# Kernel optimization log

Hardware: AMD Instinct MI355X
Metric: run time of the kernel (lower is better)

The kernel has to match this reference:

```python
import jax, jax.numpy as jnp
import numpy as np

B, T, D = 2, 2048, 2048
H = 8
KEY_DIM, VAL_DIM = 1024, 2048   # expand_k=0.5, expand_v=1.0
HK, HV = KEY_DIM // H, VAL_DIM // H
LOW_RANK = 16
GATE_NORM = 16.0
CHUNK = 64
HIDDEN = (D * 4 * 2 // 3 + 63) // 64 * 64  # 5504, exactly as GLUFFN.__init__
EPS = 1e-6


def rmsnorm(x, w):
    return x * jax.lax.rsqrt(jnp.mean(x * x, axis=-1, keepdims=True) + EPS) * w


def setup_inputs() -> dict:
    key = jax.random.key(0)
    ks = jax.random.split(key, 12)
    w = lambda k, s: jax.random.normal(k, s, jnp.float32) * 0.02
    return {
        "x": jax.random.normal(ks[0], (B, T, D), jnp.float32),
        "norm1_w": jnp.ones((D,), jnp.float32),
        "wq": w(ks[1], (D, KEY_DIM)),
        "wk": w(ks[2], (D, KEY_DIM)),
        "wv": w(ks[3], (D, VAL_DIM)),
        "gk_w1": w(ks[4], (D, LOW_RANK)),
        "gk_w2": w(ks[5], (LOW_RANK, KEY_DIM)),
        "gk_b": jnp.zeros((KEY_DIM,), jnp.float32),
        "wg": w(ks[6], (D, VAL_DIM)),
        "gnorm_w": jnp.ones((HV,), jnp.float32),
        "wo": w(ks[7], (VAL_DIM, D)),
        "ffn_norm_w": jnp.ones((D,), jnp.float32),
        "w_gate": w(ks[8], (D, HIDDEN)),
        "w_up": w(ks[9], (D, HIDDEN)),
        "w_down": w(ks[10], (HIDDEN, D)),
    }


def _gla(h, wq, wk, wv, gk_w1, gk_w2, gk_b, wg, gnorm_w, wo):
    # Gated linear attention, chunk-parallel form (fla-style):
    #   S_t = diag(exp(g_t)) S_{t-1} + k_t^T v_t ;  o_t = q_t S_t
    Bb, Tt, _ = h.shape
    nc = Tt // CHUNK

    def split(t, hd):  # [B,T,H*hd] -> [nc,B,H,CHUNK,hd]
        t = t.reshape(Bb, nc, CHUNK, H, hd)
        return jnp.transpose(t, (1, 0, 3, 2, 4))

    q = split(h @ wq, HK) * (HK ** -0.5)
    k = split(h @ wk, HK)
    v = split(h @ wv, HV)
    # low-rank forget gate, log-sigmoid scaled by gate_logit_normalizer=16
    g = split(jax.nn.log_sigmoid(h @ gk_w1 @ gk_w2 + gk_b) / GATE_NORM, HK)

    mask = jnp.tril(jnp.ones((CHUNK, CHUNK), jnp.float32))

    def step(S, inp):
        qc, kc, vc, gc = inp                       # [B,H,C,*]
        b = jnp.cumsum(gc, axis=-2)                # cumulative log-decay within chunk
        qe = qc * jnp.exp(b)
        A = jnp.einsum('bhik,bhjk->bhij', qe, kc * jnp.exp(-b)) * mask
        o = jnp.einsum('bhck,bhkv->bhcv', qe, S) + jnp.einsum('bhij,bhjv->bhiv', A, vc)
        bl = b[:, :, -1:, :]                       # decay to end of chunk
        S = jnp.exp(bl[:, :, 0, :])[..., None] * S + \
            jnp.einsum('bhck,bhcv->bhkv', kc * jnp.exp(bl - b), vc)
        return S, o

    S0 = jnp.zeros((Bb, H, HK, HV), h.dtype)
    _, o = jax.lax.scan(step, S0, (q, k, v, g))    # o: [nc,B,H,C,HV]
    o = jnp.transpose(o, (1, 0, 3, 2, 4)).reshape(Bb, Tt, H, HV)

    gate = (h @ wg).reshape(Bb, Tt, H, HV)
    # per-head RMSNorm + swish output gate (FusedRMSNormSwishGate)
    o = rmsnorm(o, gnorm_w) * gate * jax.nn.sigmoid(gate)
    return o.reshape(Bb, Tt, VAL_DIM) @ wo


def reference(x, norm1_w, wq, wk, wv, gk_w1, gk_w2, gk_b, wg, gnorm_w, wo,
              ffn_norm_w, w_gate, w_up, w_down):
    h = rmsnorm(x, norm1_w)
    x = x + _gla(h, wq, wk, wv, gk_w1, gk_w2, gk_b, wg, gnorm_w, wo)
    h2 = rmsnorm(x, ffn_norm_w)
    ffn = (jax.nn.silu(h2 @ w_gate) * (h2 @ w_up)) @ w_down  # GLUFFN, dropout=eval
    return x + ffn
```

## Files before the change

### kernel.cpp

```cpp
#include <hip/hip_runtime.h>

typedef unsigned short u16;
typedef __attribute__((ext_vector_type(8))) short bh8;
typedef __attribute__((ext_vector_type(4))) float f4;

__device__ __forceinline__ float bf2f(u16 u) {
  union { unsigned int i; float f; } x; x.i = ((unsigned int)u) << 16; return x.f;
}
__device__ __forceinline__ u16 f2bf(float f) {
  union { float f; unsigned int i; } x; x.f = f;
  unsigned int r = x.i + 0x7fffu + ((x.i >> 16) & 1u);
  return (u16)(r >> 16);
}
__device__ __forceinline__ f4 mfma16(bh8 a, bh8 b, f4 c) {
  return __builtin_amdgcn_mfma_f32_16x16x32_bf16(a, b, c, 0, 0, 0);
}
__device__ __forceinline__ void gload16(const void* g, void* l) {
  __builtin_amdgcn_global_load_lds(
      (const __attribute__((address_space(1))) void*)g,
      (__attribute__((address_space(3))) void*)l, 16, 0, 0);
}

__device__ __forceinline__ bh8 rd8(const u16* arr, int row, int col, int rowbytes) {
  return *(const bh8*)((const char*)arr + row * rowbytes + ((col * 2) ^ ((row & 7) << 4)));
}

__global__ __launch_bounds__(256)
void wtrans_k(const float* __restrict__ src, u16* __restrict__ dst, int R, int C,
              int rmul, int roff) {
  __shared__ float tile[32][33];
  int tx = threadIdx.x & 31, ty = threadIdx.x >> 5;
  int c0 = blockIdx.x * 32, r0 = blockIdx.y * 32;
#pragma unroll
  for (int yy = 0; yy < 32; yy += 8)
    tile[ty + yy][tx] = src[(size_t)(r0 + ty + yy) * C + c0 + tx];
  __syncthreads();
#pragma unroll
  for (int yy = 0; yy < 32; yy += 8)
    dst[(size_t)((c0 + ty + yy) * rmul + roff) * R + r0 + tx] = f2bf(tile[tx][ty + yy]);
}

__global__ __launch_bounds__(256)
void rmsnorm_k(const float* __restrict__ x, const float* __restrict__ w,
               u16* __restrict__ out) {
  int row = blockIdx.x, t = threadIdx.x;
  const float* xr = x + (size_t)row * 2048;
  float4 a = ((const float4*)xr)[t * 2];
  float4 b = ((const float4*)xr)[t * 2 + 1];
  float ss = a.x*a.x + a.y*a.y + a.z*a.z + a.w*a.w
           + b.x*b.x + b.y*b.y + b.z*b.z + b.w*b.w;
#pragma unroll
  for (int s = 32; s > 0; s >>= 1) ss += __shfl_xor(ss, s, 64);
  __shared__ float red[4];
  if ((t & 63) == 0) red[t >> 6] = ss;
  __syncthreads();
  float rr = rsqrtf((red[0] + red[1] + red[2] + red[3]) * (1.0f / 2048.0f) + 1e-6f);
  float v[8] = {a.x, a.y, a.z, a.w, b.x, b.y, b.z, b.w};
  int c0 = t * 8;
  u16* orow = out + (size_t)row * 2048 + c0;
#pragma unroll
  for (int j = 0; j < 8; ++j) orow[j] = f2bf(v[j] * rr * w[c0 + j]);
}

template <int EPI, typename OutT>
__global__ __launch_bounds__(512, 2)
void gemm2(const u16* __restrict__ A, const u16* __restrict__ Bt,
           OutT* __restrict__ C, void* __restrict__ aux, float scale,
           int M, int N, int K, int gx) {
  constexpr int SB = 32768;
  __shared__ char lds[3 * SB];
  int t = threadIdx.x, lane = t & 63, w = t >> 6;
  int c_ = lane & 15, r_ = lane >> 4;
  int wm = w >> 2, wn = w & 3;

  int nwg = gridDim.x;
  int wg = (blockIdx.x & 7) * (nwg >> 3) + (blockIdx.x >> 3);
  int gy = nwg / gx;
  int bx = wg / gy, by = wg % gy;
  int m0 = by * 256, n0 = bx * 256;

  const char* baseA[2];
#pragma unroll
  for (int h = 0; h < 2; ++h) {
    int p = h * 512 + t;
    int cc = p ^ ((p >> 3) & 7);
    baseA[h] = (const char*)A + ((size_t)(m0 + (cc >> 2)) * K + (cc & 3) * 8) * 2;
  }
  const char* baseB[2];
#pragma unroll
  for (int h = 0; h < 2; ++h) {
    int p = h * 512 + t;
    int cc = p ^ ((p >> 3) & 7);
    baseB[h] = (const char*)Bt + ((size_t)(n0 + (cc >> 2)) * K + (cc & 3) * 8) * 2;
  }
  int offA[8], offB[4];
#pragma unroll
  for (int mb = 0; mb < 8; ++mb) {
    int cc = (wm * 128 + mb * 16 + c_) * 4 + r_;
    offA[mb] = (cc ^ ((cc >> 3) & 7)) * 16;
  }
#pragma unroll
  for (int nb = 0; nb < 4; ++nb) {
    int cc = (wn * 64 + nb * 16 + c_) * 4 + r_;
    offB[nb] = (cc ^ ((cc >> 3) & 7)) * 16 + 16384;
  }
  int ldsW = w * 1024;

  f4 z4 = {0.f, 0.f, 0.f, 0.f};
  f4 acc[8][4];
#pragma unroll
  for (int mb = 0; mb < 8; ++mb)
#pragma unroll
    for (int nb = 0; nb < 4; ++nb) acc[mb][nb] = z4;

  int NT = K >> 5;

#define STAGEA(S, ko)                                                       \
  {                                                                         \
    _Pragma("unroll") for (int h = 0; h < 2; ++h)                           \
        gload16(baseA[h] + (ko), lds + (S) * SB + h * 8192 + ldsW);         \
  }
#define STAGEB(S, ko)                                                       \
  {                                                                         \
    _Pragma("unroll") for (int h = 0; h < 2; ++h)                           \
        gload16(baseB[h] + (ko), lds + (S) * SB + 16384 + h * 8192 + ldsW); \
  }
#define KTILE(S)                                                            \
  {                                                                         \
    int kts = kt + 2; if (kts >= NT) kts -= NT;                             \
    bh8 fb[4], fa[4], fa2[4];                                               \
    _Pragma("unroll") for (int nb = 0; nb < 4; ++nb)                        \
        fb[nb] = *(const bh8*)(lds + (S) * SB + offB[nb]);                  \
    _Pragma("unroll") for (int mb = 0; mb < 4; ++mb)                        \
        fa[mb] = *(const bh8*)(lds + (S) * SB + offA[mb]);                  \
    STAGEA(((S) + 2) % 3, kts << 6);                                        \
    asm volatile("s_waitcnt lgkmcnt(0)" ::: "memory");                      \
    __builtin_amdgcn_sched_barrier(0);                                      \
    _Pragma("unroll") for (int mb = 0; mb < 4; ++mb)                        \
        fa2[mb] = *(const bh8*)(lds + (S) * SB + offA[mb + 4]);             \
    STAGEB(((S) + 2) % 3, kts << 6);                                        \
    __builtin_amdgcn_sched_barrier(0);                                      \
    __builtin_amdgcn_s_setprio(1);                                          \
    _Pragma("unroll") for (int mb = 0; mb < 4; ++mb)                        \
        _Pragma("unroll") for (int nb = 0; nb < 4; ++nb)                    \
            acc[mb][nb] = mfma16(fa[mb], fb[nb], acc[mb][nb]);              \
    __builtin_amdgcn_s_setprio(0);                                          \
    asm volatile("s_waitcnt lgkmcnt(0)" ::: "memory");                      \
    __builtin_amdgcn_sched_barrier(0);                                      \
    __builtin_amdgcn_s_setprio(1);                                          \
    _Pragma("unroll") for (int mb = 0; mb < 4; ++mb)                        \
        _Pragma("unroll") for (int nb = 0; nb < 4; ++nb)                    \
            acc[mb + 4][nb] = mfma16(fa2[mb], fb[nb], acc[mb + 4][nb]);     \
    __builtin_amdgcn_s_setprio(0);                                          \
    __builtin_amdgcn_sched_barrier(0);                                      \
    asm volatile("s_waitcnt vmcnt(4)" ::: "memory");                        \
    __builtin_amdgcn_s_barrier();                                           \
    asm volatile("" ::: "memory");                                          \
  }

  STAGEA(0, 0); STAGEB(0, 0);
  STAGEA(1, 64); STAGEB(1, 64);
  asm volatile("s_waitcnt vmcnt(4)" ::: "memory");
  __builtin_amdgcn_s_barrier();
  asm volatile("" ::: "memory");

  int kt = 0;
  while (true) {
    KTILE(0); if (++kt == NT) break;
    KTILE(1); if (++kt == NT) break;
    KTILE(2); if (++kt == NT) break;
  }
  asm volatile("s_waitcnt vmcnt(0)" ::: "memory");
#undef KTILE
#undef STAGEA
#undef STAGEB

  int rowBase = m0 + wm * 128;
#pragma unroll
  for (int mb = 0; mb < 8; ++mb) {
#pragma unroll
    for (int rr = 0; rr < 4; ++rr) {
      int row = rowBase + mb * 16 + r_ * 4 + rr;
#pragma unroll
      for (int nb = 0; nb < 4; ++nb) {
        int col = n0 + wn * 64 + nb * 16 + c_;
        float val = acc[mb][nb][rr];
        if (EPI == 1) {
          ((float*)C)[(size_t)row * N + col] = val + ((const float*)aux)[(size_t)row * N + col];
        } else if (EPI == 5) {
          if (col < 1024) ((u16*)C)[(size_t)row * 1024 + col] = f2bf(val * scale);
          else ((u16*)aux)[(size_t)row * 1024 + col - 1024] = f2bf(val);
        } else if (EPI == 4) {
          if (col < 2048) {
            int bb = row >> 11, t2 = row & 2047;
            int pan = ((bb << 5) + (t2 >> 6)) * 8 + (col >> 8);
            int ii = t2 & 63, vv = col & 255;
            *(u16*)((char*)C + (size_t)pan * 32768 + vv * 128 + ((ii * 2) ^ ((vv & 7) << 4)))
                = f2bf(val);
          } else {
            ((u16*)aux)[(size_t)row * 2048 + col - 2048] = f2bf(val);
          }
        } else if (EPI == 6) {
          float other = __shfl_xor(val, 1, 64);
          if (lane & 1) {
            float gv = other;
            ((u16*)C)[(size_t)row * 5504 + (col >> 1)] = f2bf(val * (gv / (1.f + expf(-gv))));
          }
        }
      }
    }
  }
}

__global__ __launch_bounds__(256)
void lowrank_k(const u16* __restrict__ h, const float* __restrict__ w1,
               const float* __restrict__ w2, const float* __restrict__ bias,
               float* __restrict__ g) {
  int row = blockIdx.x, t = threadIdx.x, lane = t & 63, wave = t >> 6;
  const u16* hr = h + (size_t)row * 2048;
  bh8 hv = *(const bh8*)&hr[t * 8];
  float p[16];
#pragma unroll
  for (int j = 0; j < 16; ++j) p[j] = 0.f;
#pragma unroll
  for (int kk = 0; kk < 8; ++kk) {
    float f = bf2f((u16)hv[kk]);
    const float* wrow = w1 + (size_t)(t * 8 + kk) * 16;
#pragma unroll
    for (int j = 0; j < 16; ++j) p[j] += f * wrow[j];
  }
#pragma unroll
  for (int j = 0; j < 16; ++j)
#pragma unroll
    for (int s = 32; s > 0; s >>= 1) p[j] += __shfl_xor(p[j], s, 64);
  __shared__ float gl[4][16];
  if (lane == 0) {
#pragma unroll
    for (int j = 0; j < 16; ++j) gl[wave][j] = p[j];
  }
  __syncthreads();
  float glow[16];
#pragma unroll
  for (int j = 0; j < 16; ++j) glow[j] = gl[0][j] + gl[1][j] + gl[2][j] + gl[3][j];
  float* grow = g + (size_t)row * 1024;
#pragma unroll
  for (int nn = 0; nn < 4; ++nn) {
    int n = nn * 256 + t;
    float z = bias[n];
#pragma unroll
    for (int j = 0; j < 16; ++j) z += glow[j] * w2[j * 1024 + n];
    float ls = fminf(z, 0.f) - log1pf(expf(-fabsf(z)));
    grow[n] = ls * (1.0f / 16.0f);
  }
}

__global__ __launch_bounds__(128)
void gprep_k(u16* __restrict__ q, u16* __restrict__ k, const float* __restrict__ g,
             u16* __restrict__ keT, float* __restrict__ ebl) {
  int bid = blockIdx.x;
  int h = bid & 7, bc = bid >> 3;
  int b = bc >> 5, c = bc & 31;
  int ch = threadIdx.x;
  size_t base = ((size_t)(b * 2048 + c * 64)) * 1024 + h * 128 + ch;
  char* keTp = (char*)keT + (size_t)bid * 16384 + ch * 128;
  int sw = (ch & 7) << 4;
  float bacc = 0.f;
  for (int i8 = 0; i8 < 8; ++i8) {
    u16 kp[8];
#pragma unroll
    for (int e = 0; e < 8; ++e) {
      size_t off = base + (size_t)(i8 * 8 + e) * 1024;
      bacc += g[off];
      float eb = __expf(bacc);
      float reb = __builtin_amdgcn_rcpf(eb);
      float qv = bf2f(q[off]), kv = bf2f(k[off]);
      q[off] = f2bf(qv * eb);
      u16 kev = f2bf(kv * reb);
      k[off] = kev;
      kp[e] = kev;
    }
    *(bh8*)(keTp + ((i8 * 16) ^ sw)) = *(const bh8*)kp;
  }
  ebl[(size_t)bid * 128 + ch] = __expf(bacc);
}

__global__ __launch_bounds__(256)
void gla_scan(const u16* __restrict__ qg, const u16* __restrict__ kg,
              const u16* __restrict__ keTg, const u16* __restrict__ vTg,
              const float* __restrict__ eblg, float* __restrict__ outp) {
  __shared__ u16 qeL[64 * 128];
  __shared__ u16 keL[64 * 128];
  __shared__ u16 kTL[128 * 64];
  __shared__ u16 vTL[64 * 64];
  __shared__ u16 AL[64 * 64];
  __shared__ u16 SbL[64 * 128];
  __shared__ float SfL[64][133];

  int t = threadIdx.x, lane = t & 63, w = t >> 6;
  int vb = blockIdx.x & 3, bh = blockIdx.x >> 2;
  int b = bh >> 3, h = bh & 7;
  int c_ = lane & 15, r_ = lane >> 4;
  f4 z4 = {0.f, 0.f, 0.f, 0.f};

  for (int i = t; i < 64 * 128; i += 256) SbL[i] = 0;
  for (int i = t; i < 64 * 133; i += 256) ((float*)SfL)[i] = 0.f;

  const char* qbase = (const char*)qg + (size_t)b * 2048 * 2048 + h * 256;
  const char* kbase = (const char*)kg + (size_t)b * 2048 * 2048 + h * 256;
  int rowoff = (t >> 4) * 2048 + (t & 15) * 16;
  int4 pq[4], pk[4], pkt[4], pvt[2];

#define LOADCH(cc)                                                              \
  {                                                                             \
    const char* qc = qbase + (size_t)(cc) * 64 * 2048;                          \
    const char* kc = kbase + (size_t)(cc) * 64 * 2048;                          \
    int panel_ = ((b * 32 + (cc)) * 8 + h);                                     \
    const char* ktc = (const char*)keTg + (size_t)panel_ * 16384;               \
    const char* vtc = (const char*)vTg + (size_t)panel_ * 32768 + vb * 8192;    \
    _Pragma("unroll")                                                           \
    for (int j = 0; j < 4; ++j) {                                               \
      pq[j] = *(const int4*)(qc + j * 16 * 2048 + rowoff);                      \
      pk[j] = *(const int4*)(kc + j * 16 * 2048 + rowoff);                      \
      pkt[j] = *(const int4*)(ktc + j * 4096 + t * 16);                         \
    }                                                                           \
    _Pragma("unroll")                                                           \
    for (int j = 0; j < 2; ++j) pvt[j] = *(const int4*)(vtc + j * 4096 + t * 16); \
  }

  LOADCH(0);
  for (int c = 0; c < 32; ++c) {
#pragma unroll
    for (int j = 0; j < 4; ++j) {
      int L = j * 4096 + t * 16;
      int d = (L & ~255) | ((L & 255) ^ (((L >> 8) & 7) << 4));
      *(int4*)((char*)qeL + d) = pq[j];
      *(int4*)((char*)keL + d) = pk[j];
      *(int4*)((char*)kTL + L) = pkt[j];
    }
#pragma unroll
    for (int j = 0; j < 2; ++j) *(int4*)((char*)vTL + j * 4096 + t * 16) = pvt[j];
    if (c < 31) LOADCH(c + 1);
    int panel = ((b * 32 + c) * 8 + h);
    float eblr[2][4];
#pragma unroll
    for (int kt = 0; kt < 2; ++kt)
#pragma unroll
      for (int r = 0; r < 4; ++r)
        eblr[kt][r] = eblg[(size_t)panel * 128 + w * 32 + kt * 16 + r_ * 4 + r];
    __syncthreads();

    f4 accA[4] = {z4, z4, z4, z4};
    f4 accS[2][4] = {{z4, z4, z4, z4}, {z4, z4, z4, z4}};
#pragma unroll
    for (int ks = 0; ks < 4; ++ks) {
      bh8 a = rd8(qeL, w * 16 + c_, ks * 32 + r_ * 8, 256);
#pragma unroll
      for (int n = 0; n < 4; ++n)
        accA[n] = mfma16(a, rd8(keL, n * 16 + c_, ks * 32 + r_ * 8, 256), accA[n]);
    }
#pragma unroll
    for (int ks = 0; ks < 2; ++ks) {
      bh8 bf_[4];
#pragma unroll
      for (int n = 0; n < 4; ++n) bf_[n] = rd8(vTL, n * 16 + c_, ks * 32 + r_ * 8, 128);
#pragma unroll
      for (int kt = 0; kt < 2; ++kt) {
        bh8 a = rd8(kTL, w * 32 + kt * 16 + c_, ks * 32 + r_ * 8, 128);
#pragma unroll
        for (int n = 0; n < 4; ++n) accS[kt][n] = mfma16(a, bf_[n], accS[kt][n]);
      }
    }
#pragma unroll
    for (int n = 0; n < 4; ++n)
#pragma unroll
      for (int r = 0; r < 4; ++r) {
        int i = w * 16 + r_ * 4 + r, j = n * 16 + c_;
        *(u16*)((char*)AL + i * 128 + ((j * 2) ^ ((i & 7) << 4))) =
            (j <= i) ? f2bf(accA[n][r]) : (u16)0;
      }
    __syncthreads();

    f4 acco[4] = {z4, z4, z4, z4};
#pragma unroll
    for (int ks = 0; ks < 4; ++ks) {
      bh8 a = rd8(qeL, w * 16 + c_, ks * 32 + r_ * 8, 256);
#pragma unroll
      for (int n = 0; n < 4; ++n)
        acco[n] = mfma16(a, rd8(SbL, n * 16 + c_, ks * 32 + r_ * 8, 256), acco[n]);
    }
#pragma unroll
    for (int ks = 0; ks < 2; ++ks) {
      bh8 a = rd8(AL, w * 16 + c_, ks * 32 + r_ * 8, 128);
#pragma unroll
      for (int n = 0; n < 4; ++n)
        acco[n] = mfma16(a, rd8(vTL, n * 16 + c_, ks * 32 + r_ * 8, 128), acco[n]);
    }
    {
      size_t obase = (size_t)(b * 2048 + c * 64 + w * 16 + r_ * 4) * 2048 + h * 256 + vb * 64;
#pragma unroll
      for (int n = 0; n < 4; ++n)
#pragma unroll
        for (int r = 0; r < 4; ++r)
          outp[obase + (size_t)r * 2048 + n * 16 + c_] = acco[n][r];
    }
    __syncthreads();

#pragma unroll
    for (int kt = 0; kt < 2; ++kt)
#pragma unroll
      for (int n = 0; n < 4; ++n)
#pragma unroll
        for (int r = 0; r < 4; ++r) {
          int kk = w * 32 + kt * 16 + r_ * 4 + r;
          int vcol = n * 16 + c_;
          float nv = eblr[kt][r] * (SfL[vcol][kk] + accS[kt][n][r]);
          SfL[vcol][kk] = nv;
          *(u16*)((char*)SbL + vcol * 256 + ((kk * 2) ^ ((vcol & 7) << 4))) = f2bf(nv);
        }
    __syncthreads();
  }
#undef LOADCH
}

__global__ __launch_bounds__(256)
void ogate_k(const float* __restrict__ o, const u16* __restrict__ gate,
             const float* __restrict__ gw, u16* __restrict__ og) {
  int tok = blockIdx.x, t = threadIdx.x;
  int head = t >> 5, l32 = t & 31, v0 = l32 * 8;
  size_t base = (size_t)tok * 2048 + head * 256 + v0;
  float4 a = *(const float4*)&o[base];
  float4 b = *(const float4*)&o[base + 4];
  float ov[8] = {a.x, a.y, a.z, a.w, b.x, b.y, b.z, b.w};
  float ss = 0.f;
#pragma unroll
  for (int j = 0; j < 8; ++j) ss += ov[j] * ov[j];
#pragma unroll
  for (int s = 16; s > 0; s >>= 1) ss += __shfl_xor(ss, s, 32);
  float rr = rsqrtf(ss * (1.0f / 256.0f) + 1e-6f);
#pragma unroll
  for (int j = 0; j < 8; ++j) {
    float gv = bf2f(gate[base + j]);
    float val = ov[j] * rr * gw[v0 + j];
    og[base + j] = f2bf(val * gv / (1.f + expf(-gv)));
  }
}

extern "C" void kernel_launch(void* const* d_in, const int* in_sizes, int n_in,
                              void* d_out, int out_size, void* d_ws, size_t ws_size,
                              hipStream_t stream) {
  (void)in_sizes; (void)n_in; (void)out_size; (void)ws_size;
  const float* x = (const float*)d_in[0];
  const float* n1w = (const float*)d_in[1];
  const float* wq = (const float*)d_in[2];
  const float* wk = (const float*)d_in[3];
  const float* wv = (const float*)d_in[4];
  const float* gw1 = (const float*)d_in[5];
  const float* gw2 = (const float*)d_in[6];
  const float* gb = (const float*)d_in[7];
  const float* wg = (const float*)d_in[8];
  const float* gnw = (const float*)d_in[9];
  const float* wo = (const float*)d_in[10];
  const float* fnw = (const float*)d_in[11];
  const float* wgate = (const float*)d_in[12];
  const float* wup = (const float*)d_in[13];
  const float* wdown = (const float*)d_in[14];
  float* out = (float*)d_out;

  char* ws = (char*)d_ws;
  size_t off = 0;
  auto alloc = [&](size_t bytes) { size_t p = off; off += (bytes + 255) & ~(size_t)255; return p; };
  u16* wqT = (u16*)(ws + alloc(2ull * 1024 * 2048));
  u16* wkT = (u16*)(ws + alloc(2ull * 1024 * 2048));
  u16* wvT = (u16*)(ws + alloc(2ull * 2048 * 2048));
  u16* wgT = (u16*)(ws + alloc(2ull * 2048 * 2048));
  u16* woT = (u16*)(ws + alloc(2ull * 2048 * 2048));
  u16* btGU = (u16*)(ws + alloc(2ull * 11008 * 2048));
  u16* wdT = (u16*)(ws + alloc(2ull * 2048 * 5504));
  u16* h_bf = (u16*)(ws + alloc(2ull * 4096 * 2048));
  u16* q_bf = (u16*)(ws + alloc(2ull * 4096 * 1024));
  u16* k_bf = (u16*)(ws + alloc(2ull * 4096 * 1024));
  u16* vT_g = (u16*)(ws + alloc(2ull * 4096 * 2048));
  u16* gate_bf = (u16*)(ws + alloc(2ull * 4096 * 2048));
  float* g_f = (float*)(ws + alloc(4ull * 4096 * 1024));
  float* o_f = (float*)(ws + alloc(4ull * 4096 * 2048));
  u16* mid = (u16*)(ws + alloc(2ull * 4096 * 5504));
  float* ebl_g = (float*)(ws + alloc(4ull * 512 * 128));
  u16* keT_g = h_bf;
  u16* og = h_bf;
  u16* h2 = q_bf;
  float* x2 = o_f;

  dim3 blk(256);
  dim3 blk2(512);
  wtrans_k<<<dim3(32, 64), blk, 0, stream>>>(wq, wqT, 2048, 1024, 1, 0);
  wtrans_k<<<dim3(32, 64), blk, 0, stream>>>(wk, wkT, 2048, 1024, 1, 0);
  wtrans_k<<<dim3(64, 64), blk, 0, stream>>>(wv, wvT, 2048, 2048, 1, 0);
  wtrans_k<<<dim3(64, 64), blk, 0, stream>>>(wg, wgT, 2048, 2048, 1, 0);
  wtrans_k<<<dim3(64, 64), blk, 0, stream>>>(wo, woT, 2048, 2048, 1, 0);
  wtrans_k<<<dim3(172, 64), blk, 0, stream>>>(wgate, btGU, 2048, 5504, 2, 0);
  wtrans_k<<<dim3(172, 64), blk, 0, stream>>>(wup, btGU, 2048, 5504, 2, 1);
  wtrans_k<<<dim3(64, 172), blk, 0, stream>>>(wdown, wdT, 5504, 2048, 1, 0);

  rmsnorm_k<<<4096, blk, 0, stream>>>(x, n1w, h_bf);

  gemm2<5, u16><<<128, blk2, 0, stream>>>(h_bf, wqT, q_bf, k_bf, 0.08838834764831845f,
                                          4096, 2048, 2048, 8);
  gemm2<4, u16><<<256, blk2, 0, stream>>>(h_bf, wvT, vT_g, gate_bf, 1.f,
                                          4096, 4096, 2048, 16);
  lowrank_k<<<4096, blk, 0, stream>>>(h_bf, gw1, gw2, gb, g_f);

  gprep_k<<<512, dim3(128), 0, stream>>>(q_bf, k_bf, g_f, keT_g, ebl_g);

  gla_scan<<<64, blk, 0, stream>>>(q_bf, k_bf, keT_g, vT_g, ebl_g, o_f);

  ogate_k<<<4096, blk, 0, stream>>>(o_f, gate_bf, gnw, og);

  gemm2<1, float><<<128, blk2, 0, stream>>>(og, woT, x2, (void*)x, 1.f,
                                            4096, 2048, 2048, 8);

  rmsnorm_k<<<4096, blk, 0, stream>>>(x2, fnw, h2);

  gemm2<6, u16><<<688, blk2, 0, stream>>>(h2, btGU, mid, nullptr, 1.f,
                                          4096, 11008, 2048, 43);
  gemm2<1, float><<<128, blk2, 0, stream>>>(mid, wdT, out, x2, 1.f,
                                            4096, 2048, 5504, 8);
}
```

Measured before the change: 983.8 us.

## Prefetch next k-tile A fragments from LDS during MFMA of current tile

Restructures the GEMM main loop so the A-fragments for the next k-tile are read from LDS into a second register set while the current tile's 32 MFMAs run. The loop is unrolled six ways to ping-pong between the two register sets. Global-to-LDS staging for A and B is merged and issued at the top of each tile, and a second barrier is added per iteration. The aim is to hide LDS read latency behind matrix math, at the cost of eight extra vector registers per lane and an extra barrier.

```diff
diff --git a/kernel.cpp b/kernel.cpp
--- a/kernel.cpp
+++ b/kernel.cpp
@@ -114,66 +114,62 @@
     for (int nb = 0; nb < 4; ++nb) acc[mb][nb] = z4;
 
   int NT = K >> 5;
-
-#define STAGEA(S, ko)                                                       \
+  bh8 fa0[8], fa1[8], fbB[4];
+
+#define STAGE(S, ko)                                                        \
   {                                                                         \
     _Pragma("unroll") for (int h = 0; h < 2; ++h)                           \
         gload16(baseA[h] + (ko), lds + (S) * SB + h * 8192 + ldsW);         \
-  }
-#define STAGEB(S, ko)                                                       \
-  {                                                                         \
     _Pragma("unroll") for (int h = 0; h < 2; ++h)                           \
         gload16(baseB[h] + (ko), lds + (S) * SB + 16384 + h * 8192 + ldsW); \
   }
-#define KTILE(S)                                                            \
+#define KTILE(S, FAC, FAN)                                                  \
   {                                                                         \
     int kts = kt + 2; if (kts >= NT) kts -= NT;                             \
-    bh8 fb[4], fa[4], fa2[4];                                               \
+    constexpr int S1 = ((S) + 1) % 3, S2 = ((S) + 2) % 3;                   \
+    STAGE(S2, kts << 6);                                                    \
     _Pragma("unroll") for (int nb = 0; nb < 4; ++nb)                        \
-        fb[nb] = *(const bh8*)(lds + (S) * SB + offB[nb]);                  \
-    _Pragma("unroll") for (int mb = 0; mb < 4; ++mb)                        \
-        fa[mb] = *(const bh8*)(lds + (S) * SB + offA[mb]);                  \
-    STAGEA(((S) + 2) % 3, kts << 6);                                        \
-    asm volatile("s_waitcnt lgkmcnt(0)" ::: "memory");                      \
-    __builtin_amdgcn_sched_barrier(0);                                      \
-    _Pragma("unroll") for (int mb = 0; mb < 4; ++mb)                        \
-        fa2[mb] = *(const bh8*)(lds + (S) * SB + offA[mb + 4]);             \
-    STAGEB(((S) + 2) % 3, kts << 6);                                        \
-    __builtin_amdgcn_sched_barrier(0);                                      \
-    __builtin_amdgcn_s_setprio(1);                                          \
-    _Pragma("unroll") for (int mb = 0; mb < 4; ++mb)                        \
-        _Pragma("unroll") for (int nb = 0; nb < 4; ++nb)                    \
-            acc[mb][nb] = mfma16(fa[mb], fb[nb], acc[mb][nb]);              \
-    __builtin_amdgcn_s_setprio(0);                                          \
-    asm volatile("s_waitcnt lgkmcnt(0)" ::: "memory");                      \
-    __builtin_amdgcn_sched_barrier(0);                                      \
-    __builtin_amdgcn_s_setprio(1);                                          \
-    _Pragma("unroll") for (int mb = 0; mb < 4; ++mb)                        \
-        _Pragma("unroll") for (int nb = 0; nb < 4; ++nb)                    \
-            acc[mb + 4][nb] = mfma16(fa2[mb], fb[nb], acc[mb + 4][nb]);     \
-    __builtin_amdgcn_s_setprio(0);                                          \
+        fbB[nb] = *(const bh8*)(lds + (S) * SB + offB[nb]);                 \
     __builtin_amdgcn_sched_barrier(0);                                      \
     asm volatile("s_waitcnt vmcnt(4)" ::: "memory");                        \
     __builtin_amdgcn_s_barrier();                                           \
+    __builtin_amdgcn_sched_barrier(0);                                      \
+    _Pragma("unroll") for (int mb = 0; mb < 8; ++mb)                        \
+        FAN[mb] = *(const bh8*)(lds + S1 * SB + offA[mb]);                  \
+    __builtin_amdgcn_sched_barrier(0);                                      \
+    asm volatile("s_waitcnt lgkmcnt(8)" ::: "memory");                      \
+    __builtin_amdgcn_sched_barrier(0);                                      \
+    __builtin_amdgcn_s_setprio(1);                                          \
+    _Pragma("unroll") for (int mb = 0; mb < 8; ++mb)                        \
+        _Pragma("unroll") for (int nb = 0; nb < 4; ++nb)                    \
+            acc[mb][nb] = mfma16(FAC[mb], fbB[nb], acc[mb][nb]);            \
+    __builtin_amdgcn_s_setprio(0);                                          \
+    __builtin_amdgcn_sched_barrier(0);                                      \
+    __builtin_amdgcn_s_barrier();                                           \
     asm volatile("" ::: "memory");                                          \
   }
 
-  STAGEA(0, 0); STAGEB(0, 0);
-  STAGEA(1, 64); STAGEB(1, 64);
+  STAGE(0, 0);
+  STAGE(1, 64);
   asm volatile("s_waitcnt vmcnt(4)" ::: "memory");
   __builtin_amdgcn_s_barrier();
-  asm volatile("" ::: "memory");
+  __builtin_amdgcn_sched_barrier(0);
+#pragma unroll
+  for (int mb = 0; mb < 8; ++mb) fa0[mb] = *(const bh8*)(lds + offA[mb]);
+  __builtin_amdgcn_sched_barrier(0);
 
   int kt = 0;
   while (true) {
-    KTILE(0); if (++kt == NT) break;
-    KTILE(1); if (++kt == NT) break;
-    KTILE(2); if (++kt == NT) break;
-  }
-  asm volatile("s_waitcnt vmcnt(0)" ::: "memory");
+    KTILE(0, fa0, fa1); if (++kt == NT) break;
+    KTILE(1, fa1, fa0); if (++kt == NT) break;
+    KTILE(2, fa0, fa1); if (++kt == NT) break;
+    KTILE(0, fa1, fa0); if (++kt == NT) break;
+    KTILE(1, fa0, fa1); if (++kt == NT) break;
+    KTILE(2, fa1, fa0); if (++kt == NT) break;
+  }
+  asm volatile("s_waitcnt vmcnt(0) lgkmcnt(0)" ::: "memory");
 #undef KTILE
-#undef STAGEA
-#undef STAGEB
+#undef STAGE
 
   int rowBase = m0 + wm * 128;
 #pragma unroll
```

Measured after the change: 1.089 ms. +10.7%, slower.
